# Kernel tuning notes

Measured on AMD Instinct MI355X. Metric: run time of the kernel, lower is better.

## Reference

```python
import jax, jax.numpy as jnp
import numpy as np

T, B, C, H = 2048, 2, 1024, 16
D = C // H
SCALE = D ** -0.5
WSTD = C ** -0.5  # keep activations O(1) so softmax is not saturated


def setup_inputs() -> dict:
    key = jax.random.key(0)
    ks = jax.random.split(key, 6)
    return {
        "x": jax.random.normal(ks[0], (T, B, C), dtype=jnp.float32),
        "wq": jax.random.normal(ks[1], (C, C), dtype=jnp.float32) * WSTD,
        "wk": jax.random.normal(ks[2], (C, C), dtype=jnp.float32) * WSTD,
        "wv": jax.random.normal(ks[3], (C, C), dtype=jnp.float32) * WSTD,
        "wo": jax.random.normal(ks[4], (C, C), dtype=jnp.float32) * WSTD,
        "bo": jax.random.normal(ks[5], (C,), dtype=jnp.float32) * 0.02,
    }


def reference(x, wq, wk, wv, wo, bo):
    t, b, c = x.shape
    x2 = x.reshape(t * b, c)
    # SelfAttentionLinears: q scaled by head_dim^-0.5 inside the addmm
    q = (x2 @ wq) * SCALE
    k = x2 @ wk
    v = x2 @ wv
    # fairseq layout: (T, B*H, D) -> (B*H, T, D)
    q = q.reshape(t, b * H, D).transpose(1, 0, 2)
    k = k.reshape(t, b * H, D).transpose(1, 0, 2)
    v = v.reshape(t, b * H, D).transpose(1, 0, 2)
    # strided_bmm1: scores [B*H, T, T]
    scores = jnp.einsum('bqd,bkd->bqk', q, k)
    attn = jax.nn.softmax(scores, axis=-1)
    # strided_bmm2: context [B*H, T, D]
    ctx = jnp.einsum('bqk,bkd->bqd', attn, v)
    out = ctx.transpose(1, 0, 2).reshape(t, b, c)
    return out @ wo + bo
```

## Files before the change

### kernel.cpp

```cpp
#include <hip/hip_runtime.h>
#include <math.h>

#define T_DIM 2048
#define B_DIM 2
#define C_DIM 1024
#define H_DIM 16
#define D_DIM 64
#define M_DIM (T_DIM * B_DIM)
#define SCALE_Q 0.125f

typedef short short8 __attribute__((ext_vector_type(8)));
typedef float f32x4  __attribute__((ext_vector_type(4)));
typedef unsigned short ushort_t;

__device__ __forceinline__ unsigned short f2bf(float f) {
    unsigned int u = __builtin_bit_cast(unsigned int, f);
    u += 0x7FFFu + ((u >> 16) & 1u);
    return (unsigned short)(u >> 16);
}

__device__ __forceinline__ void gl_lds16(const void* g, void* l) {
    __builtin_amdgcn_global_load_lds(
        (const __attribute__((address_space(1))) void*)g,
        (__attribute__((address_space(3))) void*)l, 16, 0, 0);
}

__global__ __launch_bounds__(256) void cast_x(
    const float* __restrict__ x, ushort_t* __restrict__ xb)
{
    const size_t i = ((size_t)blockIdx.x * 256 + threadIdx.x) * 8;
    const float4 v0 = *(const float4*)&x[i];
    const float4 v1 = *(const float4*)&x[i + 4];
    ushort_t o[8] = {f2bf(v0.x), f2bf(v0.y), f2bf(v0.z), f2bf(v0.w),
                     f2bf(v1.x), f2bf(v1.y), f2bf(v1.z), f2bf(v1.w)};
    *(uint4*)&xb[i] = *(uint4*)o;
}

__global__ __launch_bounds__(256) void transpose_w(
    const float* __restrict__ wq, const float* __restrict__ wk,
    const float* __restrict__ wv, const float* __restrict__ wo,
    ushort_t* __restrict__ wqkv_t, ushort_t* __restrict__ wo_t)
{
    __shared__ float tile[64][65];
    const int tid = threadIdx.x;
    const int k0  = blockIdx.x * 64;
    const int n0  = blockIdx.y * 64;
    const int z   = blockIdx.z;
    const float* src = (z == 0) ? wq : (z == 1) ? wk : (z == 2) ? wv : wo;
    ushort_t* dst = (z < 3) ? (wqkv_t + (size_t)z * C_DIM * C_DIM) : wo_t;

    const int r = tid >> 4;
    const int c = (tid & 15) * 4;
#pragma unroll
    for (int i = 0; i < 4; ++i) {
        const float4 v = *(const float4*)&src[(size_t)(k0 + r + i * 16) * C_DIM + n0 + c];
        *(float4*)&tile[r + i * 16][c] = v;
    }
    __syncthreads();
#pragma unroll
    for (int i = 0; i < 4; ++i) {
        const int r2 = r + i * 16;
        ushort4 o;
        o.x = f2bf(tile[c + 0][r2]); o.y = f2bf(tile[c + 1][r2]);
        o.z = f2bf(tile[c + 2][r2]); o.w = f2bf(tile[c + 3][r2]);
        *(ushort4*)&dst[(size_t)(n0 + r2) * C_DIM + k0 + c] = o;
    }
}

__global__ __launch_bounds__(256) void qkv_mfma(
    const ushort_t* __restrict__ xb, const ushort_t* __restrict__ wt,
    ushort_t* __restrict__ q_ws, ushort_t* __restrict__ k_ws,
    ushort_t* __restrict__ v_ws)
{
    __shared__ ushort_t lds[18432];
    ushort_t* As = lds;
    ushort_t* Bs = lds + 4096;

    const int tid  = threadIdx.x;
    const int n0   = blockIdx.x * 128;
    const int m0   = blockIdx.y * 128;
    const int w    = tid >> 6;
    const int lane = tid & 63;
    const int l16  = lane & 15;
    const int quad = lane >> 4;
    const int wm   = (w >> 1) * 64;
    const int wn   = (w & 1) * 64;

    const int o0 = tid * 8, o1 = o0 + 2048;
    const ushort_t* a0 = xb + (size_t)(m0 + (o0 >> 5)) * C_DIM + (o0 & 31);
    const ushort_t* a1 = xb + (size_t)(m0 + (o1 >> 5)) * C_DIM + (o1 & 31);
    const ushort_t* b0 = wt + (size_t)(n0 + (o0 >> 5)) * C_DIM + (o0 & 31);
    const ushort_t* b1 = wt + (size_t)(n0 + (o1 >> 5)) * C_DIM + (o1 & 31);

    f32x4 acc[4][4] = {};

    for (int k0 = 0; k0 < C_DIM; k0 += 32) {
        __syncthreads();
        gl_lds16(a0 + k0, As + o0);
        gl_lds16(a1 + k0, As + o1);
        gl_lds16(b0 + k0, Bs + o0);
        gl_lds16(b1 + k0, Bs + o1);
        __syncthreads();

        short8 af[4], bf[4];
#pragma unroll
        for (int mi = 0; mi < 4; ++mi)
            af[mi] = *(const short8*)&As[(wm + mi * 16 + l16) * 32 + quad * 8];
#pragma unroll
        for (int ni = 0; ni < 4; ++ni)
            bf[ni] = *(const short8*)&Bs[(wn + ni * 16 + l16) * 32 + quad * 8];
#pragma unroll
        for (int mi = 0; mi < 4; ++mi)
#pragma unroll
            for (int ni = 0; ni < 4; ++ni)
                acc[mi][ni] = __builtin_amdgcn_mfma_f32_16x16x32_bf16(
                    af[mi], bf[ni], acc[mi][ni], 0, 0, 0);
    }

    __syncthreads();
    ushort_t* Ep = lds + w * 4608;

    const int mat = n0 >> 10;
    const int cb  = (n0 & 1023) + wn;
    const int h   = cb >> 6;
    ushort_t* dst = (mat == 0) ? q_ws : (mat == 1) ? k_ws : v_ws;
    const float sc = (mat == 0) ? SCALE_Q : 1.0f;

#pragma unroll
    for (int mi = 0; mi < 4; ++mi)
#pragma unroll
        for (int ni = 0; ni < 4; ++ni)
#pragma unroll
            for (int r = 0; r < 4; ++r)
                Ep[(mi * 16 + quad * 4 + r) * 72 + ni * 16 + l16] =
                    f2bf(acc[mi][ni][r] * sc);

    const int rq = lane >> 3;
    const int c8 = (lane & 7) * 8;
#pragma unroll
    for (int p = 0; p < 8; ++p) {
        const int row = p * 8 + rq;
        const uint4 val = *(const uint4*)&Ep[row * 72 + c8];
        const int m = m0 + wm + row;
        const int t = m >> 1, b = m & 1;
        *(uint4*)&dst[((size_t)(b * H_DIM + h) * T_DIM + t) * D_DIM + c8] = val;
    }
}

__global__ __launch_bounds__(256) void v_transpose(
    const ushort_t* __restrict__ vn, ushort_t* __restrict__ vt)
{
    __shared__ ushort_t tile[64][72];
    const int tid = threadIdx.x;
    const int t0  = blockIdx.x * 64;
    const int bh  = blockIdx.y;
    const int r   = tid >> 3;
    const int c   = (tid & 7) * 8;
#pragma unroll
    for (int i = 0; i < 2; ++i)
        *(uint4*)&tile[r + i * 32][c] =
            *(const uint4*)&vn[((size_t)bh * T_DIM + t0 + r + i * 32) * D_DIM + c];
    __syncthreads();
#pragma unroll
    for (int i = 0; i < 2; ++i) {
        const int rd = r + i * 32;
        ushort_t o[8];
#pragma unroll
        for (int j = 0; j < 8; ++j) o[j] = tile[c + j][rd];
        *(uint4*)&vt[((size_t)bh * D_DIM + rd) * T_DIM + t0 + c] = *(uint4*)o;
    }
}

__global__ __launch_bounds__(256) void attn_mfma(
    const ushort_t* __restrict__ q, const ushort_t* __restrict__ k,
    const ushort_t* __restrict__ v, ushort_t* __restrict__ ctx)
{
    __shared__ ushort_t Ks [64][88];
    __shared__ ushort_t Vts[64][88];
    __shared__ ushort_t Ps [64][88];

    const int tid  = threadIdx.x;
    const int bh   = blockIdx.x;
    const int q0   = blockIdx.y * 64;
    const int w    = tid >> 6;
    const int lane = tid & 63;
    const int l16  = lane & 15;
    const int quad = lane >> 4;

    const int r0 = tid >> 3,         c80 = (tid & 7) * 8;
    const int r1 = (tid + 256) >> 3, c81 = c80;
    const ushort_t* kbase = k + (size_t)bh * T_DIM * D_DIM;
    const ushort_t* vbase = v + (size_t)bh * D_DIM * T_DIM;

    short8 aq0, aq1;
    {
        const ushort_t* qrow = q + ((size_t)bh * T_DIM + q0 + 16 * w + l16) * D_DIM;
        aq0 = *(const short8*)(qrow + quad * 8);
        aq1 = *(const short8*)(qrow + 32 + quad * 8);
    }

    f32x4 O[4] = {};
    float lacc[4] = {0.f, 0.f, 0.f, 0.f};

    uint4 kr0 = *(const uint4*)(kbase + (size_t)r0 * D_DIM + c80);
    uint4 kr1 = *(const uint4*)(kbase + (size_t)r1 * D_DIM + c81);
    uint4 vr0 = *(const uint4*)(vbase + (size_t)r0 * T_DIM + c80);
    uint4 vr1 = *(const uint4*)(vbase + (size_t)r1 * T_DIM + c81);

    const float LOG2E = 1.44269504f;
    const float SHIFT = 8.0f * 1.44269504f;

    for (int kt = 0; kt < 32; ++kt) {
        __syncthreads();
        *(uint4*)&Ks[r0][c80]  = kr0;
        *(uint4*)&Ks[r1][c81]  = kr1;
        *(uint4*)&Vts[r0][c80] = vr0;
        *(uint4*)&Vts[r1][c81] = vr1;
        if (kt + 1 < 32) {
            const int kn = (kt + 1) * 64;
            kr0 = *(const uint4*)(kbase + (size_t)(kn + r0) * D_DIM + c80);
            kr1 = *(const uint4*)(kbase + (size_t)(kn + r1) * D_DIM + c81);
            vr0 = *(const uint4*)(vbase + (size_t)r0 * T_DIM + kn + c80);
            vr1 = *(const uint4*)(vbase + (size_t)r1 * T_DIM + kn + c81);
        }
        __syncthreads();

        f32x4 S[4];
#pragma unroll
        for (int nt = 0; nt < 4; ++nt) {
            const short8 b0 = *(const short8*)&Ks[nt * 16 + l16][quad * 8];
            const short8 b1 = *(const short8*)&Ks[nt * 16 + l16][32 + quad * 8];
            f32x4 s = (f32x4){0.f, 0.f, 0.f, 0.f};
            s = __builtin_amdgcn_mfma_f32_16x16x32_bf16(aq0, b0, s, 0, 0, 0);
            s = __builtin_amdgcn_mfma_f32_16x16x32_bf16(aq1, b1, s, 0, 0, 0);
            S[nt] = s;
        }

#pragma unroll
        for (int nt = 0; nt < 4; ++nt)
#pragma unroll
            for (int r = 0; r < 4; ++r) {
                const float p = exp2f(fmaf(S[nt][r], LOG2E, -SHIFT));
                lacc[r] += p;
                Ps[16 * w + quad * 4 + r][nt * 16 + l16] =
                    (ushort_t)(__builtin_bit_cast(unsigned int, p) >> 16);
            }

        const short8 ap0 = *(const short8*)&Ps[16 * w + l16][quad * 8];
        const short8 ap1 = *(const short8*)&Ps[16 * w + l16][32 + quad * 8];
#pragma unroll
        for (int nt = 0; nt < 4; ++nt) {
            const short8 b0 = *(const short8*)&Vts[nt * 16 + l16][quad * 8];
            const short8 b1 = *(const short8*)&Vts[nt * 16 + l16][32 + quad * 8];
            O[nt] = __builtin_amdgcn_mfma_f32_16x16x32_bf16(ap0, b0, O[nt], 0, 0, 0);
            O[nt] = __builtin_amdgcn_mfma_f32_16x16x32_bf16(ap1, b1, O[nt], 0, 0, 0);
        }
    }

#pragma unroll
    for (int r = 0; r < 4; ++r) {
        float s = lacc[r];
        s += __shfl_xor(s, 1);
        s += __shfl_xor(s, 2);
        s += __shfl_xor(s, 4);
        s += __shfl_xor(s, 8);
        lacc[r] = s;
    }

    const int b = bh >> 4;
    const int h = bh & 15;
#pragma unroll
    for (int r = 0; r < 4; ++r) {
        const float inv = 1.0f / lacc[r];
        const int row = q0 + 16 * w + quad * 4 + r;
#pragma unroll
        for (int nt = 0; nt < 4; ++nt)
            ctx[((size_t)row * B_DIM + b) * C_DIM + h * 64 + nt * 16 + l16] =
                f2bf(O[nt][r] * inv);
    }
}

__global__ __launch_bounds__(256) void out_mfma(
    const ushort_t* __restrict__ ctx, const ushort_t* __restrict__ wot,
    const float* __restrict__ bo, float* __restrict__ out)
{
    __shared__ ushort_t As[128 * 32];
    __shared__ ushort_t Bs[64 * 32];

    const int tid  = threadIdx.x;
    const int n0   = blockIdx.x * 64;
    const int m0   = blockIdx.y * 128;
    const int w    = tid >> 6;
    const int lane = tid & 63;
    const int l16  = lane & 15;
    const int quad = lane >> 4;
    const int wm   = (w >> 1) * 64;
    const int wn   = (w & 1) * 32;

    const int o0 = tid * 8, o1 = o0 + 2048;
    const ushort_t* a0 = ctx + (size_t)(m0 + (o0 >> 5)) * C_DIM + (o0 & 31);
    const ushort_t* a1 = ctx + (size_t)(m0 + (o1 >> 5)) * C_DIM + (o1 & 31);
    const ushort_t* b0 = wot + (size_t)(n0 + (o0 >> 5)) * C_DIM + (o0 & 31);

    f32x4 acc[4][2] = {};

    for (int k0 = 0; k0 < C_DIM; k0 += 32) {
        __syncthreads();
        gl_lds16(a0 + k0, As + o0);
        gl_lds16(a1 + k0, As + o1);
        gl_lds16(b0 + k0, Bs + o0);
        __syncthreads();

        short8 af[4], bf[2];
#pragma unroll
        for (int mi = 0; mi < 4; ++mi)
            af[mi] = *(const short8*)&As[(wm + mi * 16 + l16) * 32 + quad * 8];
#pragma unroll
        for (int ni = 0; ni < 2; ++ni)
            bf[ni] = *(const short8*)&Bs[(wn + ni * 16 + l16) * 32 + quad * 8];
#pragma unroll
        for (int mi = 0; mi < 4; ++mi)
#pragma unroll
            for (int ni = 0; ni < 2; ++ni)
                acc[mi][ni] = __builtin_amdgcn_mfma_f32_16x16x32_bf16(
                    af[mi], bf[ni], acc[mi][ni], 0, 0, 0);
    }

#pragma unroll
    for (int ni = 0; ni < 2; ++ni) {
        const int n = n0 + wn + ni * 16 + l16;
        const float bias = bo[n];
#pragma unroll
        for (int mi = 0; mi < 4; ++mi) {
            const int mb = m0 + wm + mi * 16 + quad * 4;
#pragma unroll
            for (int r = 0; r < 4; ++r)
                out[(size_t)(mb + r) * C_DIM + n] = acc[mi][ni][r] + bias;
        }
    }
}

extern "C" void kernel_launch(void* const* d_in, const int* in_sizes, int n_in,
                              void* d_out, int out_size, void* d_ws, size_t ws_size,
                              hipStream_t stream)
{
    const float* x  = (const float*)d_in[0];
    const float* wq = (const float*)d_in[1];
    const float* wk = (const float*)d_in[2];
    const float* wv = (const float*)d_in[3];
    const float* wo = (const float*)d_in[4];
    const float* bo = (const float*)d_in[5];
    float* out = (float*)d_out;

    const size_t CC  = (size_t)C_DIM * C_DIM;
    const size_t MC  = (size_t)M_DIM * C_DIM;
    ushort_t* xb     = (ushort_t*)d_ws;
    ushort_t* wqkv_t = xb + MC;
    ushort_t* wo_t   = wqkv_t + 3 * CC;
    ushort_t* q_ws   = wo_t + CC;
    ushort_t* k_ws   = q_ws + MC;
    ushort_t* v_nat  = k_ws + MC;
    ushort_t* v_t    = v_nat + MC;
    ushort_t* ctx    = v_t + MC;

    hipLaunchKernelGGL(cast_x, dim3(2048), dim3(256), 0, stream, x, xb);
    hipLaunchKernelGGL(transpose_w, dim3(16, 16, 4), dim3(256), 0, stream,
                       wq, wk, wv, wo, wqkv_t, wo_t);
    hipLaunchKernelGGL(qkv_mfma, dim3(24, 32), dim3(256), 0, stream,
                       xb, wqkv_t, q_ws, k_ws, v_nat);
    hipLaunchKernelGGL(v_transpose, dim3(32, 32), dim3(256), 0, stream,
                       v_nat, v_t);
    hipLaunchKernelGGL(attn_mfma, dim3(32, 32), dim3(256), 0, stream,
                       q_ws, k_ws, v_t, ctx);
    hipLaunchKernelGGL(out_mfma, dim3(16, 32), dim3(256), 0, stream,
                       ctx, wo_t, bo, out);
}
```

Measured before the change: 214.1 us.

## Merge cast and weight transpose kernels, compute softmax row sums via MFMA

Measured after the change: 212.7 us. Within noise of the previous version (-0.7%).

```diff
diff --git a/kernel.cpp b/kernel.cpp
--- a/kernel.cpp
+++ b/kernel.cpp
@@ -25,27 +25,34 @@
         (__attribute__((address_space(3))) void*)l, 16, 0, 0);
 }
 
-__global__ __launch_bounds__(256) void cast_x(
-    const float* __restrict__ x, ushort_t* __restrict__ xb)
-{
-    const size_t i = ((size_t)blockIdx.x * 256 + threadIdx.x) * 8;
-    const float4 v0 = *(const float4*)&x[i];
-    const float4 v1 = *(const float4*)&x[i + 4];
-    ushort_t o[8] = {f2bf(v0.x), f2bf(v0.y), f2bf(v0.z), f2bf(v0.w),
-                     f2bf(v1.x), f2bf(v1.y), f2bf(v1.z), f2bf(v1.w)};
-    *(uint4*)&xb[i] = *(uint4*)o;
-}
-
-__global__ __launch_bounds__(256) void transpose_w(
+__global__ __launch_bounds__(256) void prep(
+    const float* __restrict__ x,
     const float* __restrict__ wq, const float* __restrict__ wk,
     const float* __restrict__ wv, const float* __restrict__ wo,
+    ushort_t* __restrict__ xb,
     ushort_t* __restrict__ wqkv_t, ushort_t* __restrict__ wo_t)
 {
     __shared__ float tile[64][65];
     const int tid = threadIdx.x;
-    const int k0  = blockIdx.x * 64;
-    const int n0  = blockIdx.y * 64;
     const int z   = blockIdx.z;
+
+    if (z == 4) {
+        const size_t base =
+            ((size_t)(blockIdx.y * 16 + blockIdx.x)) * 16384 + (size_t)tid * 8;
+#pragma unroll
+        for (int j = 0; j < 8; ++j) {
+            const size_t i = base + (size_t)j * 2048;
+            const float4 v0 = *(const float4*)&x[i];
+            const float4 v1 = *(const float4*)&x[i + 4];
+            ushort_t o[8] = {f2bf(v0.x), f2bf(v0.y), f2bf(v0.z), f2bf(v0.w),
+                             f2bf(v1.x), f2bf(v1.y), f2bf(v1.z), f2bf(v1.w)};
+            *(uint4*)&xb[i] = *(uint4*)o;
+        }
+        return;
+    }
+
+    const int k0 = blockIdx.x * 64;
+    const int n0 = blockIdx.y * 64;
     const float* src = (z == 0) ? wq : (z == 1) ? wk : (z == 2) ? wv : wo;
     ushort_t* dst = (z < 3) ? (wqkv_t + (size_t)z * C_DIM * C_DIM) : wo_t;
 
@@ -175,9 +182,9 @@
     const ushort_t* __restrict__ q, const ushort_t* __restrict__ k,
     const ushort_t* __restrict__ v, ushort_t* __restrict__ ctx)
 {
-    __shared__ ushort_t Ks [64][88];
-    __shared__ ushort_t Vts[64][88];
-    __shared__ ushort_t Ps [64][88];
+    __shared__ ushort_t Ks [64][72];
+    __shared__ ushort_t Vts[64][72];
+    __shared__ ushort_t Ps [64][72];
 
     const int tid  = threadIdx.x;
     const int bh   = blockIdx.x;
@@ -188,7 +195,7 @@
     const int quad = lane >> 4;
 
     const int r0 = tid >> 3,         c80 = (tid & 7) * 8;
-    const int r1 = (tid + 256) >> 3, c81 = c80;
+    const int r1 = (tid + 256) >> 3;
     const ushort_t* kbase = k + (size_t)bh * T_DIM * D_DIM;
     const ushort_t* vbase = v + (size_t)bh * D_DIM * T_DIM;
 
@@ -199,13 +206,21 @@
         aq1 = *(const short8*)(qrow + 32 + quad * 8);
     }
 
+    short8 vones;
+#pragma unroll
+    for (int j = 0; j < 8; ++j) vones[j] = (short)0x3F80;
+
     f32x4 O[4] = {};
-    float lacc[4] = {0.f, 0.f, 0.f, 0.f};
-
-    uint4 kr0 = *(const uint4*)(kbase + (size_t)r0 * D_DIM + c80);
-    uint4 kr1 = *(const uint4*)(kbase + (size_t)r1 * D_DIM + c81);
-    uint4 vr0 = *(const uint4*)(vbase + (size_t)r0 * T_DIM + c80);
-    uint4 vr1 = *(const uint4*)(vbase + (size_t)r1 * T_DIM + c81);
+    f32x4 Osum = {};
+
+    const ushort_t* kp0 = kbase + (size_t)r0 * D_DIM + c80;
+    const ushort_t* kp1 = kbase + (size_t)r1 * D_DIM + c80;
+    const ushort_t* vp0 = vbase + (size_t)r0 * T_DIM + c80;
+    const ushort_t* vp1 = vbase + (size_t)r1 * T_DIM + c80;
+    uint4 kr0 = *(const uint4*)kp0;  kp0 += 64 * D_DIM;
+    uint4 kr1 = *(const uint4*)kp1;  kp1 += 64 * D_DIM;
+    uint4 vr0 = *(const uint4*)vp0;  vp0 += 64;
+    uint4 vr1 = *(const uint4*)vp1;  vp1 += 64;
 
     const float LOG2E = 1.44269504f;
     const float SHIFT = 8.0f * 1.44269504f;
@@ -213,15 +228,14 @@
     for (int kt = 0; kt < 32; ++kt) {
         __syncthreads();
         *(uint4*)&Ks[r0][c80]  = kr0;
-        *(uint4*)&Ks[r1][c81]  = kr1;
+        *(uint4*)&Ks[r1][c80]  = kr1;
         *(uint4*)&Vts[r0][c80] = vr0;
-        *(uint4*)&Vts[r1][c81] = vr1;
+        *(uint4*)&Vts[r1][c80] = vr1;
         if (kt + 1 < 32) {
-            const int kn = (kt + 1) * 64;
-            kr0 = *(const uint4*)(kbase + (size_t)(kn + r0) * D_DIM + c80);
-            kr1 = *(const uint4*)(kbase + (size_t)(kn + r1) * D_DIM + c81);
-            vr0 = *(const uint4*)(vbase + (size_t)r0 * T_DIM + kn + c80);
-            vr1 = *(const uint4*)(vbase + (size_t)r1 * T_DIM + kn + c81);
+            kr0 = *(const uint4*)kp0;  kp0 += 64 * D_DIM;
+            kr1 = *(const uint4*)kp1;  kp1 += 64 * D_DIM;
+            vr0 = *(const uint4*)vp0;  vp0 += 64;
+            vr1 = *(const uint4*)vp1;  vp1 += 64;
         }
         __syncthreads();
 
@@ -240,14 +254,17 @@
         for (int nt = 0; nt < 4; ++nt)
 #pragma unroll
             for (int r = 0; r < 4; ++r) {
-                const float p = exp2f(fmaf(S[nt][r], LOG2E, -SHIFT));
-                lacc[r] += p;
-                Ps[16 * w + quad * 4 + r][nt * 16 + l16] =
-                    (ushort_t)(__builtin_bit_cast(unsigned int, p) >> 16);
+                union { float f; ushort2 h; } cv;
+                cv.f = exp2f(fmaf(S[nt][r], LOG2E, -SHIFT));
+                Ps[16 * w + quad * 4 + r][nt * 16 + l16] = cv.h.y;
             }
 
         const short8 ap0 = *(const short8*)&Ps[16 * w + l16][quad * 8];
         const short8 ap1 = *(const short8*)&Ps[16 * w + l16][32 + quad * 8];
+
+        Osum = __builtin_amdgcn_mfma_f32_16x16x32_bf16(ap0, vones, Osum, 0, 0, 0);
+        Osum = __builtin_amdgcn_mfma_f32_16x16x32_bf16(ap1, vones, Osum, 0, 0, 0);
+
 #pragma unroll
         for (int nt = 0; nt < 4; ++nt) {
             const short8 b0 = *(const short8*)&Vts[nt * 16 + l16][quad * 8];
@@ -257,21 +274,11 @@
         }
     }
 
-#pragma unroll
-    for (int r = 0; r < 4; ++r) {
-        float s = lacc[r];
-        s += __shfl_xor(s, 1);
-        s += __shfl_xor(s, 2);
-        s += __shfl_xor(s, 4);
-        s += __shfl_xor(s, 8);
-        lacc[r] = s;
-    }
-
     const int b = bh >> 4;
     const int h = bh & 15;
 #pragma unroll
     for (int r = 0; r < 4; ++r) {
-        const float inv = 1.0f / lacc[r];
+        const float inv = 1.0f / Osum[r];
         const int row = q0 + 16 * w + quad * 4 + r;
 #pragma unroll
         for (int nt = 0; nt < 4; ++nt)
@@ -363,9 +370,8 @@
     ushort_t* v_t    = v_nat + MC;
     ushort_t* ctx    = v_t + MC;
 
-    hipLaunchKernelGGL(cast_x, dim3(2048), dim3(256), 0, stream, x, xb);
-    hipLaunchKernelGGL(transpose_w, dim3(16, 16, 4), dim3(256), 0, stream,
-                       wq, wk, wv, wo, wqkv_t, wo_t);
+    hipLaunchKernelGGL(prep, dim3(16, 16, 5), dim3(256), 0, stream,
+                       x, wq, wk, wv, wo, xb, wqkv_t, wo_t);
     hipLaunchKernelGGL(qkv_mfma, dim3(24, 32), dim3(256), 0, stream,
                        xb, wqkv_t, q_ws, k_ws, v_nat);
     hipLaunchKernelGGL(v_transpose, dim3(32, 32), dim3(256), 0, stream,
```
